# Performance work log

Hardware: AMD Instinct MI355X
Metric: run time of the kernel (lower is better)

Reference implementation:

```python
import jax, jax.numpy as jnp
import numpy as np

N_HEAD = 16
HEAD_SIZE = 64  # n_embd // n_head = 1024 // 16


def setup_inputs() -> dict:
    key = jax.random.key(0)
    k1, k2 = jax.random.split(key)
    B, T, C = 2, 2048, 1024
    x = jax.random.normal(k1, (B, T, C), dtype=jnp.float32)
    w_attn = jax.random.normal(k2, (C, 3 * C), dtype=jnp.float32) * (C ** -0.5)
    b_attn = jnp.zeros((3 * C,), dtype=jnp.float32)
    return {"x": x, "w_attn": w_attn, "b_attn": b_attn}


def reference(x, w_attn, b_attn):
    B, T, C = x.shape
    qkv = x @ w_attn + b_attn  # [B, T, 3C]
    q, k, v = jnp.split(qkv, 3, axis=-1)
    # [B, T, H, D] -> [B, H, T, D]
    def heads(t):
        return t.reshape(B, T, N_HEAD, HEAD_SIZE).transpose(0, 2, 1, 3)
    q, k, v = heads(q), heads(k), heads(v)
    scale = HEAD_SIZE ** -0.5
    wei = jnp.einsum('bhqd,bhkd->bhqk', q, k) * scale  # [B, H, T, T]
    causal = jnp.tril(jnp.ones((T, T), dtype=bool))
    wei = jnp.where(causal, wei, -jnp.inf)
    wei = jax.nn.softmax(wei, axis=-1)
    out = jnp.einsum('bhqk,bhkd->bhqd', wei, v)  # [B, H, T, D]
    out = out.transpose(0, 2, 1, 3).reshape(B, T, C)
    return out
```

## Files before the change

### kernel.cpp

```cpp
#include <hip/hip_runtime.h>
#include <hip/hip_bf16.h>

#define BSZ 2
#define SEQ 2048
#define CDIM 1024
#define NHEAD 16
#define HDIM 64
#define M_GEMM (BSZ * SEQ)
#define N_GEMM (3 * CDIM)
#define K_GEMM CDIM
#define QK_PITCH (2 * CDIM)

typedef __attribute__((ext_vector_type(8))) short short8;
typedef __attribute__((ext_vector_type(4))) short short4v;
typedef __attribute__((ext_vector_type(4))) float f32x4;

__device__ __forceinline__ short bf16_rn(float f) {
    unsigned u = __builtin_bit_cast(unsigned, f);
    u += 0x7FFF + ((u >> 16) & 1);
    return (short)(u >> 16);
}

__device__ __forceinline__ void gl2lds16(const short* g, short* l) {
    __builtin_amdgcn_global_load_lds(
        (const __attribute__((address_space(1))) unsigned int*)g,
        (__attribute__((address_space(3))) unsigned int*)l, 16, 0, 0);
}

__global__ __launch_bounds__(256) void cvt_fused(const float* __restrict__ X,
                                                 const float* __restrict__ W,
                                                 short* __restrict__ Xb,
                                                 short* __restrict__ WT) {
    const int tid = threadIdx.x;
    if (blockIdx.x < 2048) {
        size_t idx = ((size_t)blockIdx.x * 256 + tid) * 8;
        float4 a = *(const float4*)&X[idx];
        float4 b = *(const float4*)&X[idx + 4];
        short8 o;
        o[0] = bf16_rn(a.x); o[1] = bf16_rn(a.y); o[2] = bf16_rn(a.z); o[3] = bf16_rn(a.w);
        o[4] = bf16_rn(b.x); o[5] = bf16_rn(b.y); o[6] = bf16_rn(b.z); o[7] = bf16_rn(b.w);
        *(short8*)&Xb[idx] = o;
        return;
    }
    __shared__ short T[64][72];
    const int bid = blockIdx.x - 2048;
    const int n0 = (bid % 48) * 64;
    const int k0 = (bid / 48) * 64;
#pragma unroll
    for (int pass = 0; pass < 4; ++pass) {
        int i = pass * 256 + tid;
        int kr = i >> 4;
        int n4 = i & 15;
        float4 v = *(const float4*)&W[(size_t)(k0 + kr) * N_GEMM + n0 + n4 * 4];
        T[n4 * 4 + 0][kr] = bf16_rn(v.x);
        T[n4 * 4 + 1][kr] = bf16_rn(v.y);
        T[n4 * 4 + 2][kr] = bf16_rn(v.z);
        T[n4 * 4 + 3][kr] = bf16_rn(v.w);
    }
    __syncthreads();
#pragma unroll
    for (int pass = 0; pass < 2; ++pass) {
        int o = pass * 256 + tid;
        int nr = o >> 3;
        int c8 = o & 7;
        *(short8*)&WT[(size_t)(n0 + nr) * K_GEMM + k0 + c8 * 8] =
            *(const short8*)&T[nr][c8 * 8];
    }
}

#define GBK 64

__global__ __launch_bounds__(256) void qkv_gemm_mfma(const short* __restrict__ A,
                                                     const short* __restrict__ Bt,
                                                     const float* __restrict__ bias,
                                                     short* __restrict__ Yqk,
                                                     short* __restrict__ Yv) {
    __shared__ short Asl[128 * GBK];
    __shared__ short Bsl[128 * GBK];

    const int tid = threadIdx.x;
    const int w = tid >> 6;
    const int l16 = tid & 15;
    const int quad = (tid & 63) >> 4;
    const int wm = w >> 1, wn = w & 1;
    const int m0 = blockIdx.y * 128;
    const int n0 = blockIdx.x * 128;

    f32x4 acc[4][4];
#pragma unroll
    for (int i = 0; i < 4; ++i)
#pragma unroll
        for (int j = 0; j < 4; ++j) acc[i][j] = (f32x4){0.f, 0.f, 0.f, 0.f};

    int arow[4], gofs[4];
#pragma unroll
    for (int p = 0; p < 4; ++p) {
        int cid = p * 256 + tid;
        arow[p] = cid >> 3;
        gofs[p] = ((cid & 7) ^ (arow[p] & 7)) * 8;
    }
    const int fsw = l16 & 7;

    for (int kt = 0; kt < K_GEMM; kt += GBK) {
        __syncthreads();
#pragma unroll
        for (int p = 0; p < 4; ++p) {
            gl2lds16(A + (size_t)(m0 + arow[p]) * K_GEMM + kt + gofs[p],
                     &Asl[(p * 256 + w * 64) * 8]);
            gl2lds16(Bt + (size_t)(n0 + arow[p]) * K_GEMM + kt + gofs[p],
                     &Bsl[(p * 256 + w * 64) * 8]);
        }
        __syncthreads();

        short8 af[4][2], bfr[4][2];
#pragma unroll
        for (int i = 0; i < 4; ++i) {
            int ra = wm * 64 + i * 16 + l16;
            int rb = wn * 64 + i * 16 + l16;
#pragma unroll
            for (int ks = 0; ks < 2; ++ks) {
                af[i][ks] = *(const short8*)&Asl[(ra * 8 + ((ks * 4 + quad) ^ fsw)) * 8];
                bfr[i][ks] = *(const short8*)&Bsl[(rb * 8 + ((ks * 4 + quad) ^ fsw)) * 8];
            }
        }
#pragma unroll
        for (int i = 0; i < 4; ++i)
#pragma unroll
            for (int j = 0; j < 4; ++j)
#pragma unroll
                for (int ks = 0; ks < 2; ++ks)
                    acc[i][j] = __builtin_amdgcn_mfma_f32_16x16x32_bf16(
                        af[i][ks], bfr[j][ks], acc[i][j], 0, 0, 0);
    }

    if (n0 >= 2 * CDIM) {
#pragma unroll
        for (int i = 0; i < 4; ++i) {
            int row0 = m0 + wm * 64 + i * 16 + quad * 4;
#pragma unroll
            for (int j = 0; j < 4; ++j) {
                int colg = n0 + wn * 64 + j * 16 + l16;
                float bb = bias[colg];
                short4v pk;
#pragma unroll
                for (int r = 0; r < 4; ++r) pk[r] = bf16_rn(acc[i][j][r] + bb);
                *(short4v*)&Yv[(size_t)(colg - 2 * CDIM) * M_GEMM + row0] = pk;
            }
        }
    } else {
        const float qs = (n0 < CDIM) ? 0.125f * 1.44269504f : 1.0f;
#pragma unroll
        for (int i = 0; i < 4; ++i)
#pragma unroll
            for (int r = 0; r < 4; ++r) {
                int row = m0 + wm * 64 + i * 16 + quad * 4 + r;
#pragma unroll
                for (int j = 0; j < 4; ++j) {
                    int colg = n0 + wn * 64 + j * 16 + l16;
                    Yqk[(size_t)row * QK_PITCH + colg] =
                        bf16_rn((acc[i][j][r] + bias[colg]) * qs);
                }
            }
    }
}

__global__ __launch_bounds__(256) void attn_mfma(const short* __restrict__ qk,
                                                 const short* __restrict__ vT,
                                                 float* __restrict__ out) {
    const int b = blockIdx.z;
    const int h = blockIdx.y;
    const int bx = blockIdx.x;
    const int u = h + 16 * b;
    const int band = u >> 3;
    const int base = (band & 2) ? ((bx + 16) & 31) : bx;
    const int qt = (band & 1) ? (31 - base) : base;
    const int tid = threadIdx.x;
    const int w = tid >> 6;
    const int lane = tid & 63;
    const int quad = lane >> 4;
    const int l16 = lane & 15;
    const int q0 = qt * 64;

    __shared__ short Ks[2][64 * 64];
    __shared__ short Vt[2][64 * 64];
    __shared__ short Ps[4 * 16 * 64];

    int koff[2], voff[2], ldso[2];
#pragma unroll
    for (int p = 0; p < 2; ++p) {
        int cid = p * 256 + w * 64 + lane;
        int row = cid >> 3;
        int c = (cid & 7) ^ (row & 7);
        koff[p] = row * QK_PITCH + c * 8;
        voff[p] = row * M_GEMM + c * 8;
        ldso[p] = (p * 256 + w * 64) * 8;
    }

    const short* qrow = qk + (size_t)(b * SEQ + q0 + w * 16 + l16) * QK_PITCH + h * HDIM;
    short8 aq[2];
    aq[0] = *(const short8*)(qrow + quad * 8);
    aq[1] = *(const short8*)(qrow + 32 + quad * 8);

    float l_run[4] = {0.f, 0.f, 0.f, 0.f};
    f32x4 o_acc[4];
#pragma unroll
    for (int dt = 0; dt < 4; ++dt) o_acc[dt] = (f32x4){0.f, 0.f, 0.f, 0.f};

    const int rowg0 = q0 + w * 16 + quad * 4;
    const short* kb0 = qk + (size_t)(b * SEQ) * QK_PITCH + CDIM + h * HDIM;
    const short* vb0 = vT + (size_t)(h * HDIM) * M_GEMM + b * SEQ;

    const int ksl = l16 & 7;
    short* PsW = &Ps[w * 1024];

#pragma unroll
    for (int p = 0; p < 2; ++p) {
        gl2lds16(kb0 + koff[p], &Ks[0][ldso[p]]);
        gl2lds16(vb0 + voff[p], &Vt[0][ldso[p]]);
    }
    __syncthreads();

    for (int kt = 0; kt <= qt; ++kt) {
        const int cur = kt & 1;

        if (kt < qt) {
            const short* kbase = kb0 + (size_t)(kt + 1) * 64 * QK_PITCH;
            const short* vbase = vb0 + (kt + 1) * 64;
#pragma unroll
            for (int p = 0; p < 2; ++p) {
                gl2lds16(kbase + koff[p], &Ks[cur ^ 1][ldso[p]]);
                gl2lds16(vbase + voff[p], &Vt[cur ^ 1][ldso[p]]);
            }
        }

        const short* KsC = Ks[cur];
        const short* VtC = Vt[cur];

        f32x4 s[4];
#pragma unroll
        for (int nt = 0; nt < 4; ++nt) s[nt] = (f32x4){0.f, 0.f, 0.f, 0.f};
#pragma unroll
        for (int nt = 0; nt < 4; ++nt)
#pragma unroll
            for (int ks = 0; ks < 2; ++ks) {
                short8 bk = *(const short8*)&KsC[(nt * 16 + l16) * 64 +
                                                 ((ks * 4 + quad) ^ ksl) * 8];
                s[nt] = __builtin_amdgcn_mfma_f32_16x16x32_bf16(aq[ks], bk, s[nt], 0, 0, 0);
            }

        if (kt < qt) {
#pragma unroll
            for (int r = 0; r < 4; ++r) {
                const int qr = quad * 4 + r;
                float lsum = 0.f;
#pragma unroll
                for (int nt = 0; nt < 4; ++nt) {
                    float pp = __builtin_amdgcn_exp2f(s[nt][r]);
                    lsum += pp;
                    int slot = (nt * 2 + (l16 >> 3)) ^ (qr & 7);
                    PsW[qr * 64 + slot * 8 + (l16 & 7)] = bf16_rn(pp);
                }
                l_run[r] += lsum;
            }
        } else {
            const int keyb = kt * 64 + l16;
#pragma unroll
            for (int r = 0; r < 4; ++r) {
                const int qr = quad * 4 + r;
                const int rowg = rowg0 + r;
                float lsum = 0.f;
#pragma unroll
                for (int nt = 0; nt < 4; ++nt) {
                    float pp = __builtin_amdgcn_exp2f(s[nt][r]);
                    pp = ((keyb + nt * 16) > rowg) ? 0.f : pp;
                    lsum += pp;
                    int slot = (nt * 2 + (l16 >> 3)) ^ (qr & 7);
                    PsW[qr * 64 + slot * 8 + (l16 & 7)] = bf16_rn(pp);
                }
                l_run[r] += lsum;
            }
        }

#pragma unroll
        for (int dt = 0; dt < 4; ++dt)
#pragma unroll
            for (int ks = 0; ks < 2; ++ks) {
                short8 ap = *(const short8*)&PsW[l16 * 64 + ((ks * 4 + quad) ^ ksl) * 8];
                short8 bv = *(const short8*)&VtC[(dt * 16 + l16) * 64 +
                                                 ((ks * 4 + quad) ^ ksl) * 8];
                o_acc[dt] = __builtin_amdgcn_mfma_f32_16x16x32_bf16(ap, bv, o_acc[dt], 0, 0, 0);
            }

        __syncthreads();
    }

#pragma unroll
    for (int r = 0; r < 4; ++r) {
        float l = l_run[r];
#pragma unroll
        for (int off = 1; off < 16; off <<= 1)
            l += __shfl_xor(l, off);
        float inv = 1.f / l;
        int row = q0 + w * 16 + quad * 4 + r;
        float* optr = out + (size_t)(b * SEQ + row) * CDIM + h * HDIM;
#pragma unroll
        for (int dt = 0; dt < 4; ++dt)
            optr[dt * 16 + l16] = o_acc[dt][r] * inv;
    }
}

extern "C" void kernel_launch(void* const* d_in, const int* in_sizes, int n_in,
                              void* d_out, int out_size, void* d_ws, size_t ws_size,
                              hipStream_t stream) {
    const float* x      = (const float*)d_in[0];
    const float* w_attn = (const float*)d_in[1];
    const float* b_attn = (const float*)d_in[2];
    float* out = (float*)d_out;

    short* qk  = (short*)d_ws;
    short* vT  = (short*)((char*)d_ws + 16777216);
    short* xb  = (short*)((char*)d_ws + 25165824);
    short* wT  = (short*)((char*)d_ws + 33554432);

    cvt_fused<<<2048 + 768, 256, 0, stream>>>(x, w_attn, xb, wT);

    dim3 g1(N_GEMM / 128, M_GEMM / 128);
    qkv_gemm_mfma<<<g1, 256, 0, stream>>>(xb, wT, b_attn, qk, vT);

    dim3 g2(SEQ / 64, NHEAD, BSZ);
    attn_mfma<<<g2, 256, 0, stream>>>(qk, vT, out);
}
```

Before: 165.7 us.

## Rewrite QKV GEMM as 256x256 tiles with double-buffered phased loads

Replaces the 128x128 single-buffered QKV GEMM with a 512-thread kernel that computes 256x256 tiles. Global-to-LDS loads for the next K tile are issued in four phases, interleaved with MFMA compute on the current buffer, using explicit vmcnt waits, raw barriers and s_setprio around the MFMA bursts. Block indices are remapped so tiles are grouped by XCD for L2 locality. This aims to hide memory latency and raise data reuse per tile. The cost is much more LDS (128 KB per block), more registers, and only 192 blocks, which may leave CUs underused.

```diff
diff --git a/kernel.cpp b/kernel.cpp
--- a/kernel.cpp
+++ b/kernel.cpp
@@ -26,6 +26,15 @@
         (const __attribute__((address_space(1))) unsigned int*)g,
         (__attribute__((address_space(3))) unsigned int*)l, 16, 0, 0);
 }
+
+#define WAITV4() asm volatile("s_waitcnt vmcnt(4)" ::: "memory")
+#define WAITV0() asm volatile("s_waitcnt vmcnt(0)" ::: "memory")
+#define SBAR()                                  \
+    do {                                        \
+        asm volatile("" ::: "memory");          \
+        __builtin_amdgcn_s_barrier();           \
+        asm volatile("" ::: "memory");          \
+    } while (0)
 
 __global__ __launch_bounds__(256) void cvt_fused(const float* __restrict__ X,
                                                  const float* __restrict__ W,
@@ -68,97 +77,191 @@
     }
 }
 
-#define GBK 64
-
-__global__ __launch_bounds__(256) void qkv_gemm_mfma(const short* __restrict__ A,
-                                                     const short* __restrict__ Bt,
-                                                     const float* __restrict__ bias,
-                                                     short* __restrict__ Yqk,
-                                                     short* __restrict__ Yv) {
-    __shared__ short Asl[128 * GBK];
-    __shared__ short Bsl[128 * GBK];
-
-    const int tid = threadIdx.x;
-    const int w = tid >> 6;
-    const int l16 = tid & 15;
-    const int quad = (tid & 63) >> 4;
-    const int wm = w >> 1, wn = w & 1;
-    const int m0 = blockIdx.y * 128;
-    const int n0 = blockIdx.x * 128;
-
-    f32x4 acc[4][4];
-#pragma unroll
-    for (int i = 0; i < 4; ++i)
+__global__ __launch_bounds__(512, 2) void qkv_gemm_8ph(const short* __restrict__ A,
+                                                       const short* __restrict__ Bt,
+                                                       const float* __restrict__ bias,
+                                                       short* __restrict__ Yqk,
+                                                       short* __restrict__ Yv) {
+    __shared__ short Asl[32768];
+    __shared__ short Bsl[32768];
+
+    const int tid  = threadIdx.x;
+    const int w    = tid >> 6;
+    const int lane = tid & 63;
+    const int l16  = lane & 15;
+    const int quad = lane >> 4;
+    const int wm   = w >> 2;
+    const int wn   = w & 3;
+    const int ls   = lane >> 3;
+    const int lc   = lane & 7;
+    const int fsw  = l16 & 7;
+
+    const int orig = blockIdx.y * 12 + blockIdx.x;
+    const int xcd  = orig & 7;
+    const int idx  = orig >> 3;
+    const int bM   = ((xcd & 1) << 3) + (idx & 7);
+    const int bN   = (xcd >> 1) * 3 + (idx >> 3);
+    const int m0   = bM << 8;
+    const int n0   = bN << 8;
+
+    const short* Ab = A  + (size_t)m0 * K_GEMM;
+    const short* Bb = Bt + (size_t)n0 * K_GEMM;
+
+    f32x4 acc[8][4];
+#pragma unroll
+    for (int i = 0; i < 8; ++i)
 #pragma unroll
         for (int j = 0; j < 4; ++j) acc[i][j] = (f32x4){0.f, 0.f, 0.f, 0.f};
 
-    int arow[4], gofs[4];
-#pragma unroll
-    for (int p = 0; p < 4; ++p) {
-        int cid = p * 256 + tid;
-        arow[p] = cid >> 3;
-        gofs[p] = ((cid & 7) ^ (arow[p] & 7)) * 8;
-    }
-    const int fsw = l16 & 7;
-
-    for (int kt = 0; kt < K_GEMM; kt += GBK) {
-        __syncthreads();
-#pragma unroll
-        for (int p = 0; p < 4; ++p) {
-            gl2lds16(A + (size_t)(m0 + arow[p]) * K_GEMM + kt + gofs[p],
-                     &Asl[(p * 256 + w * 64) * 8]);
-            gl2lds16(Bt + (size_t)(n0 + arow[p]) * K_GEMM + kt + gofs[p],
-                     &Bsl[(p * 256 + w * 64) * 8]);
+    auto stageA = [&](int unit, int tt, int sbuf) {
+#pragma unroll
+        for (int i = 0; i < 2; ++i) {
+            const int u0 = (i * 8 + w) * 8;
+            const int tr = (u0 & 63) + ((u0 >> 6) << 7) + unit * 64;
+            gl2lds16(Ab + (size_t)(tr + ls) * K_GEMM + tt * 64 + ((lc ^ ls) << 3),
+                     &Asl[sbuf * 16384 + tr * 64]);
         }
-        __syncthreads();
-
-        short8 af[4][2], bfr[4][2];
-#pragma unroll
-        for (int i = 0; i < 4; ++i) {
-            int ra = wm * 64 + i * 16 + l16;
-            int rb = wn * 64 + i * 16 + l16;
-#pragma unroll
-            for (int ks = 0; ks < 2; ++ks) {
-                af[i][ks] = *(const short8*)&Asl[(ra * 8 + ((ks * 4 + quad) ^ fsw)) * 8];
-                bfr[i][ks] = *(const short8*)&Bsl[(rb * 8 + ((ks * 4 + quad) ^ fsw)) * 8];
-            }
+    };
+    auto stageB = [&](int unit, int tt, int sbuf) {
+#pragma unroll
+        for (int i = 0; i < 2; ++i) {
+            const int u0 = (i * 8 + w) * 8;
+            const int tr = (u0 & 31) + ((u0 >> 5) << 6) + unit * 32;
+            gl2lds16(Bb + (size_t)(tr + ls) * K_GEMM + tt * 64 + ((lc ^ ls) << 3),
+                     &Bsl[sbuf * 16384 + tr * 64]);
         }
-#pragma unroll
-        for (int i = 0; i < 4; ++i)
-#pragma unroll
-            for (int j = 0; j < 4; ++j)
+    };
+    auto rdA = [&](int ab, int mi, int ks) -> short8 {
+        const int r = wm * 128 + mi * 16 + l16;
+        return *(const short8*)&Asl[ab + r * 64 + ((ks * 4 + quad) ^ fsw) * 8];
+    };
+    auto rdB = [&](int ab, int ni, int ks) -> short8 {
+        const int r = wn * 64 + ni * 16 + l16;
+        return *(const short8*)&Bsl[ab + r * 64 + ((ks * 4 + quad) ^ fsw) * 8];
+    };
+
+    stageA(0, 0, 0);
+    stageB(0, 0, 0);
+    stageB(1, 0, 0);
+    stageA(1, 0, 0);
+    WAITV4();
+    SBAR();
+
+    for (int t = 0; t < 16; ++t) {
+        const int buf = t & 1;
+        const int sb  = buf ^ 1;
+        const int tn  = (t + 1) & 15;
+        const int ab  = buf * 16384;
+
+        short8 Af[4][2], Bf[2][2];
+
+        stageA(0, tn, sb);
+#pragma unroll
+        for (int mi = 0; mi < 4; ++mi)
+#pragma unroll
+            for (int ks = 0; ks < 2; ++ks) Af[mi][ks] = rdA(ab, mi, ks);
+#pragma unroll
+        for (int ni = 0; ni < 2; ++ni)
+#pragma unroll
+            for (int ks = 0; ks < 2; ++ks) Bf[ni][ks] = rdB(ab, ni, ks);
+        __builtin_amdgcn_s_setprio(1);
+#pragma unroll
+        for (int mi = 0; mi < 4; ++mi)
+#pragma unroll
+            for (int ni = 0; ni < 2; ++ni)
 #pragma unroll
                 for (int ks = 0; ks < 2; ++ks)
-                    acc[i][j] = __builtin_amdgcn_mfma_f32_16x16x32_bf16(
-                        af[i][ks], bfr[j][ks], acc[i][j], 0, 0, 0);
-    }
+                    acc[mi][ni] = __builtin_amdgcn_mfma_f32_16x16x32_bf16(
+                        Af[mi][ks], Bf[ni][ks], acc[mi][ni], 0, 0, 0);
+        __builtin_amdgcn_s_setprio(0);
+        WAITV4();
+        SBAR();
+
+        stageB(0, tn, sb);
+#pragma unroll
+        for (int ni = 0; ni < 2; ++ni)
+#pragma unroll
+            for (int ks = 0; ks < 2; ++ks) Bf[ni][ks] = rdB(ab, 2 + ni, ks);
+        __builtin_amdgcn_s_setprio(1);
+#pragma unroll
+        for (int mi = 0; mi < 4; ++mi)
+#pragma unroll
+            for (int ni = 0; ni < 2; ++ni)
+#pragma unroll
+                for (int ks = 0; ks < 2; ++ks)
+                    acc[mi][2 + ni] = __builtin_amdgcn_mfma_f32_16x16x32_bf16(
+                        Af[mi][ks], Bf[ni][ks], acc[mi][2 + ni], 0, 0, 0);
+        __builtin_amdgcn_s_setprio(0);
+        WAITV4();
+        SBAR();
+
+        stageB(1, tn, sb);
+#pragma unroll
+        for (int mi = 0; mi < 4; ++mi)
+#pragma unroll
+            for (int ks = 0; ks < 2; ++ks) Af[mi][ks] = rdA(ab, 4 + mi, ks);
+#pragma unroll
+        for (int ni = 0; ni < 2; ++ni)
+#pragma unroll
+            for (int ks = 0; ks < 2; ++ks) Bf[ni][ks] = rdB(ab, ni, ks);
+        __builtin_amdgcn_s_setprio(1);
+#pragma unroll
+        for (int mi = 0; mi < 4; ++mi)
+#pragma unroll
+            for (int ni = 0; ni < 2; ++ni)
+#pragma unroll
+                for (int ks = 0; ks < 2; ++ks)
+                    acc[4 + mi][ni] = __builtin_amdgcn_mfma_f32_16x16x32_bf16(
+                        Af[mi][ks], Bf[ni][ks], acc[4 + mi][ni], 0, 0, 0);
+        __builtin_amdgcn_s_setprio(0);
+        SBAR();
+
+        stageA(1, tn, sb);
+#pragma unroll
+        for (int ni = 0; ni < 2; ++ni)
+#pragma unroll
+            for (int ks = 0; ks < 2; ++ks) Bf[ni][ks] = rdB(ab, 2 + ni, ks);
+        __builtin_amdgcn_s_setprio(1);
+#pragma unroll
+        for (int mi = 0; mi < 4; ++mi)
+#pragma unroll
+            for (int ni = 0; ni < 2; ++ni)
+#pragma unroll
+                for (int ks = 0; ks < 2; ++ks)
+                    acc[4 + mi][2 + ni] = __builtin_amdgcn_mfma_f32_16x16x32_bf16(
+                        Af[mi][ks], Bf[ni][ks], acc[4 + mi][2 + ni], 0, 0, 0);
+        __builtin_amdgcn_s_setprio(0);
+        WAITV4();
+        SBAR();
+    }
+    WAITV0();
 
     if (n0 >= 2 * CDIM) {
 #pragma unroll
-        for (int i = 0; i < 4; ++i) {
-            int row0 = m0 + wm * 64 + i * 16 + quad * 4;
-#pragma unroll
-            for (int j = 0; j < 4; ++j) {
-                int colg = n0 + wn * 64 + j * 16 + l16;
+        for (int mi = 0; mi < 8; ++mi) {
+            int row0 = m0 + wm * 128 + mi * 16 + quad * 4;
+#pragma unroll
+            for (int ni = 0; ni < 4; ++ni) {
+                int colg = n0 + wn * 64 + ni * 16 + l16;
                 float bb = bias[colg];
                 short4v pk;
 #pragma unroll
-                for (int r = 0; r < 4; ++r) pk[r] = bf16_rn(acc[i][j][r] + bb);
+                for (int r = 0; r < 4; ++r) pk[r] = bf16_rn(acc[mi][ni][r] + bb);
                 *(short4v*)&Yv[(size_t)(colg - 2 * CDIM) * M_GEMM + row0] = pk;
             }
         }
     } else {
         const float qs = (n0 < CDIM) ? 0.125f * 1.44269504f : 1.0f;
 #pragma unroll
-        for (int i = 0; i < 4; ++i)
+        for (int mi = 0; mi < 8; ++mi)
 #pragma unroll
             for (int r = 0; r < 4; ++r) {
-                int row = m0 + wm * 64 + i * 16 + quad * 4 + r;
-#pragma unroll
-                for (int j = 0; j < 4; ++j) {
-                    int colg = n0 + wn * 64 + j * 16 + l16;
+                int row = m0 + wm * 128 + mi * 16 + quad * 4 + r;
+#pragma unroll
+                for (int ni = 0; ni < 4; ++ni) {
+                    int colg = n0 + wn * 64 + ni * 16 + l16;
                     Yqk[(size_t)row * QK_PITCH + colg] =
-                        bf16_rn((acc[i][j][r] + bias[colg]) * qs);
+                        bf16_rn((acc[mi][ni][r] + bias[colg]) * qs);
                 }
             }
     }
@@ -324,8 +427,8 @@
 
     cvt_fused<<<2048 + 768, 256, 0, stream>>>(x, w_attn, xb, wT);
 
-    dim3 g1(N_GEMM / 128, M_GEMM / 128);
-    qkv_gemm_mfma<<<g1, 256, 0, stream>>>(xb, wT, b_attn, qk, vT);
+    dim3 g1(N_GEMM / 256, M_GEMM / 256);
+    qkv_gemm_8ph<<<g1, 512, 0, stream>>>(xb, wT, b_attn, qk, vT);
 
     dim3 g2(SEQ / 64, NHEAD, BSZ);
     attn_mfma<<<g2, 256, 0, stream>>>(qk, vT, out);
```

New measurement: 173.0 us. 4.4% more time.
